# Optimization experiments

Measured on AMD Instinct MI355X. Metric: run time of the kernel, lower is better.

Reference implementation:

```python
import jax, jax.numpy as jnp
import numpy as np

VOCAB, EMB, NDIM, B, T = 50000, 300, 512, 128, 128


def gru_cell(x, h, Wih, Whh, bih, bhh):
    # torch nn.GRU gate order: [r, z, n]
    gi = x @ Wih.T + bih
    gh = h @ Whh.T + bhh
    i_r, i_z, i_n = jnp.split(gi, 3, axis=-1)
    h_r, h_z, h_n = jnp.split(gh, 3, axis=-1)
    r = jax.nn.sigmoid(i_r + h_r)
    z = jax.nn.sigmoid(i_z + h_z)
    n = jnp.tanh(i_n + r * h_n)
    return (1.0 - z) * n + z * h


def masked_gru(X, mask, h0, Wih, Whh, bih, bhh):
    # X: T x B x d, mask: T x B, h0: B x n. Replicates _gru_forward:
    # step-0 output is stored UNmasked (o_tm1 is None), later steps blend.
    h_raw = gru_cell(X[0], h0, Wih, Whh, bih, bhh)
    m0 = mask[0][:, None]
    h = h_raw * m0 + h0 * (1.0 - m0)
    o = h_raw

    def step(carry, inp):
        h, o = carry
        x_t, m_t = inp
        m = m_t[:, None]
        hr = gru_cell(x_t, h, Wih, Whh, bih, bhh)
        h_new = hr * m + h * (1.0 - m)
        o_new = hr * m + o * (1.0 - m)
        return (h_new, o_new), o_new

    (h_f, _), o_rest = jax.lax.scan(step, (h, o), (X[1:], mask[1:]))
    return jnp.concatenate([o[None], o_rest], axis=0), h_f


def rte_forward(premise, hypothesis, E, p_Wih, p_Whh, p_bih, p_bhh,
                h_Wih, h_Whh, h_bih, h_bhh, m_Wih, m_Whh, m_bih, m_bhh,
                W_y, W_h, W_r, W_alpha, out_W, out_b):
    bsz = premise.shape[0]
    n_dim = W_y.shape[0]
    mask_p = (premise != 0).astype(E.dtype).T            # T x B
    mask_h = (hypothesis != 0).astype(E.dtype).T
    enc_p = E[premise].transpose(1, 0, 2)                # T x B x EMB (eval: no dropout)
    enc_h = E[hypothesis].transpose(1, 0, 2)
    h0 = jnp.zeros((bsz, n_dim), dtype=E.dtype)
    o_p, h_n = masked_gru(enc_p, mask_p, h0, p_Wih, p_Whh, p_bih, p_bhh)
    o_h, _ = masked_gru(enc_h, mask_h, h_n, h_Wih, h_Whh, h_bih, h_bhh)

    Y = o_p.transpose(1, 0, 2)                           # B x Tp x n
    Yw = Y @ W_y                                         # hoisted: constant across steps
    maskY = mask_p.T                                     # B x Tp

    def step(r, inp):
        h_t, m_t = inp
        s = h_t @ W_h + r @ W_r                          # B x n
        M = jnp.tanh(Yw + s[:, None, :])                 # B x Tp x n
        alpha = (M @ W_alpha)[..., 0]                    # B x Tp
        alpha = alpha - 1000.0 * (1.0 - maskY)
        alpha = jax.nn.softmax(alpha, axis=-1)
        a = jnp.einsum('bt,btn->bn', alpha, Y)
        m_in = jnp.concatenate([a, h_t], axis=-1)        # B x 2n
        rr = gru_cell(m_in, r, m_Wih, m_Whh, m_bih, m_bhh)
        m = m_t[:, None]
        r_new = rr * m + r * (1.0 - m)
        return r_new, alpha

    r0 = jnp.zeros((bsz, n_dim), dtype=E.dtype)
    r_f, _alpha_vec = jax.lax.scan(step, r0, (o_h, mask_h))
    logits = r_f @ out_W.T + out_b                       # B x 3
    return jax.nn.log_softmax(logits, axis=-1)


def setup_inputs():
    key = jax.random.key(0)
    ks = jax.random.split(key, 22)
    s = 0.05
    def rn(k, sh):
        return jax.random.normal(k, sh, dtype=jnp.float32) * s
    G = 3 * NDIM
    return {
        "premise": jax.random.randint(ks[0], (B, T), 0, VOCAB),
        "hypothesis": jax.random.randint(ks[1], (B, T), 0, VOCAB),
        "E": rn(ks[2], (VOCAB, EMB)),
        "p_Wih": rn(ks[3], (G, EMB)), "p_Whh": rn(ks[4], (G, NDIM)),
        "p_bih": rn(ks[5], (G,)), "p_bhh": rn(ks[6], (G,)),
        "h_Wih": rn(ks[7], (G, EMB)), "h_Whh": rn(ks[8], (G, NDIM)),
        "h_bih": rn(ks[9], (G,)), "h_bhh": rn(ks[10], (G,)),
        "m_Wih": rn(ks[11], (G, 2 * NDIM)), "m_Whh": rn(ks[12], (G, NDIM)),
        "m_bih": rn(ks[13], (G,)), "m_bhh": rn(ks[14], (G,)),
        "W_y": rn(ks[15], (NDIM, NDIM)), "W_h": rn(ks[16], (NDIM, NDIM)),
        "W_r": rn(ks[17], (NDIM, NDIM)), "W_alpha": rn(ks[18], (NDIM, 1)),
        "out_W": rn(ks[19], (3, NDIM)), "out_b": rn(ks[20], (3,)),
    }


def reference(premise, hypothesis, E, p_Wih, p_Whh, p_bih, p_bhh,
              h_Wih, h_Whh, h_bih, h_bhh, m_Wih, m_Whh, m_bih, m_bhh,
              W_y, W_h, W_r, W_alpha, out_W, out_b):
    return rte_forward(premise, hypothesis, E, p_Wih, p_Whh, p_bih, p_bhh,
                       h_Wih, h_Whh, h_bih, h_bhh, m_Wih, m_Whh, m_bih, m_bhh,
                       W_y, W_h, W_r, W_alpha, out_W, out_b)
```

## Files before the change

kernel.cpp:

```cpp
#include <hip/hip_runtime.h>
#include <math.h>

#define B_SZ 128
#define T_SZ 128
#define EMBD 300
#define ND 512
#define G3 1536
#define FPAD 32
#define NFID 320
#define NREP 8

typedef short s16x8 __attribute__((ext_vector_type(8)));
typedef float f32x4 __attribute__((ext_vector_type(4)));
typedef unsigned long long u64;

__device__ __forceinline__ unsigned short f2b(float x) {
    unsigned u = __float_as_uint(x);
    unsigned r = (u + 0x7fff + ((u >> 16) & 1)) >> 16;
    return (unsigned short)r;
}
__device__ __forceinline__ float b2f(unsigned short v) {
    return __uint_as_float(((unsigned)v) << 16);
}
__device__ __forceinline__ float fsigmoid(float x) { return 1.0f / (1.0f + __expf(-x)); }
__device__ __forceinline__ float ftanh(float x) { return 1.0f - 2.0f / (__expf(2.0f * x) + 1.0f); }

__device__ __forceinline__ f32x4 mfma16(s16x8 a, s16x8 b, f32x4 c) {
    return __builtin_amdgcn_mfma_f32_16x16x32_bf16(a, b, c, 0, 0, 0);
}

__device__ __forceinline__ u64 cld64(const void* p) {
    return __hip_atomic_load((const u64*)p, __ATOMIC_RELAXED, __HIP_MEMORY_SCOPE_AGENT);
}
__device__ __forceinline__ void cst64(void* p, u64 v) {
    __hip_atomic_store((u64*)p, v, __ATOMIC_RELAXED, __HIP_MEMORY_SCOPE_AGENT);
}
__device__ __forceinline__ unsigned cld32(const void* p) {
    return __hip_atomic_load((const unsigned*)p, __ATOMIC_RELAXED, __HIP_MEMORY_SCOPE_AGENT);
}
__device__ __forceinline__ void cst32(void* p, unsigned v) {
    __hip_atomic_store((unsigned*)p, v, __ATOMIC_RELAXED, __HIP_MEMORY_SCOPE_AGENT);
}
__device__ __forceinline__ s16x8 cld_frag(const unsigned short* p) {
    union { u64 q[2]; s16x8 v; } u;
    u.q[0] = cld64(p);
    u.q[1] = cld64(p + 4);
    return u.v;
}

__device__ __forceinline__ void postflag(unsigned* flags, int base, int id, unsigned ep)
{
    if (threadIdx.x < NREP)
        cst32(&flags[((long)threadIdx.x * NFID + base + id) * FPAD], ep);
}
__device__ __forceinline__ void waitflags(const unsigned* flags, int base, int n,
                                          unsigned ep, int rep)
{
    const unsigned* fr = flags + (long)rep * NFID * FPAD;
    if (threadIdx.x < 64) {
#pragma unroll 1
        for (int i = threadIdx.x; i < n; i += 64)
            while (cld32(&fr[(long)(base + i) * FPAD]) < ep)
                __builtin_amdgcn_s_sleep(2);
    }
    __syncthreads();
}
__device__ __forceinline__ void fbar(unsigned* flags, int base, int nb, unsigned ep)
{
    __syncthreads();
    postflag(flags, base, blockIdx.x & 63, ep);
    waitflags(flags, base, nb, ep, blockIdx.x & 7);
}

#define FB_GRUP 0
#define FB_GRUH 64
#define FB_LF   128
#define FB_UF   256
#define FB_SF   288

template<typename AT, bool OB>
__global__ __launch_bounds__(256)
void mfma_gemm(const AT* __restrict__ A, const int* __restrict__ idxA,
               const unsigned short* __restrict__ Wb, const float* __restrict__ bias,
               void* __restrict__ Cv,
               int M, int N, int K, int ldA, int Kpad, int ldC, int permC)
{
    __shared__ unsigned short As[64][40];
    __shared__ unsigned short Bs[64][40];
    const int tid = threadIdx.x;
    const int wv = tid >> 6, lane = tid & 63;
    const int wm = wv >> 1, wn = wv & 1;
    const int m0 = blockIdx.y * 64, n0 = blockIdx.x * 64;

    f32x4 acc[2][2] = {{{0.f,0.f,0.f,0.f},{0.f,0.f,0.f,0.f}},
                       {{0.f,0.f,0.f,0.f},{0.f,0.f,0.f,0.f}}};
    const int r_st = tid >> 2, k_st = (tid & 3) * 8;

    long arow = -1;
    {
        int gm = m0 + r_st;
        if (gm < M) arow = idxA ? (long)idxA[gm] : (long)gm;
    }

    const int kIters = (K + 31) / 32;
    for (int it = 0; it < kIters; ++it) {
        const int kg = it * 32 + k_st;
        {
            s16x8 pk = {0,0,0,0,0,0,0,0};
            if (arow >= 0) {
                if constexpr (sizeof(AT) == 2) {
                    if (kg + 8 <= K) {
                        pk = *(const s16x8*)((const unsigned short*)A + arow * (long)ldA + kg);
                    } else {
#pragma unroll
                        for (int j = 0; j < 8; ++j)
                            if (kg + j < K) pk[j] = (short)((const unsigned short*)A)[arow * (long)ldA + kg + j];
                    }
                } else {
                    if (kg + 8 <= K) {
                        const float* p = (const float*)A + arow * (long)ldA + kg;
                        f32x4 u0 = *(const f32x4*)p;
                        f32x4 u1 = *(const f32x4*)(p + 4);
#pragma unroll
                        for (int j = 0; j < 4; ++j) { pk[j] = (short)f2b(u0[j]); pk[4+j] = (short)f2b(u1[j]); }
                    } else {
#pragma unroll
                        for (int j = 0; j < 8; ++j) {
                            int kk = kg + j;
                            if (kk < K) pk[j] = (short)f2b(((const float*)A)[arow * (long)ldA + kk]);
                        }
                    }
                }
            }
            *(s16x8*)&As[r_st][k_st] = pk;
        }
        {
            int gn = n0 + r_st;
            s16x8 pk = {0,0,0,0,0,0,0,0};
            if (gn < N) pk = *(const s16x8*)&Wb[(long)gn * Kpad + kg];
            *(s16x8*)&Bs[r_st][k_st] = pk;
        }
        __syncthreads();
        {
            const int koff = (lane >> 4) * 8;
            s16x8 af[2], bfr[2];
#pragma unroll
            for (int f = 0; f < 2; ++f) {
                af[f]  = *(s16x8*)&As[wm * 32 + f * 16 + (lane & 15)][koff];
                bfr[f] = *(s16x8*)&Bs[wn * 32 + f * 16 + (lane & 15)][koff];
            }
#pragma unroll
            for (int fi = 0; fi < 2; ++fi)
#pragma unroll
                for (int fj = 0; fj < 2; ++fj)
                    acc[fi][fj] = mfma16(af[fi], bfr[fj], acc[fi][fj]);
        }
        __syncthreads();
    }
#pragma unroll
    for (int fi = 0; fi < 2; ++fi)
#pragma unroll
        for (int fj = 0; fj < 2; ++fj)
#pragma unroll
            for (int r = 0; r < 4; ++r) {
                int m = m0 + wm * 32 + fi * 16 + (lane >> 4) * 4 + r;
                int n = n0 + wn * 32 + fj * 16 + (lane & 15);
                if (m < M && n < N) {
                    float v = acc[fi][fj][r];
                    if (bias) v += bias[n];
                    long mo = permC ? ((long)(m & 127) * B_SZ + (m >> 7)) : (long)m;
                    if constexpr (OB) ((unsigned short*)Cv)[mo * ldC + n] = f2b(v);
                    else               ((float*)Cv)[mo * ldC + n] = v;
                }
            }
}

#define GRU_NB 64
__global__ __launch_bounds__(256, 1)
void gru_chain(const unsigned short* __restrict__ Whh_b, const float* __restrict__ GI,
               const float* __restrict__ bhh, const int* __restrict__ toks,
               float* __restrict__ h32,
               unsigned short* __restrict__ h16a, unsigned short* __restrict__ h16b,
               unsigned short* __restrict__ o_bt,
               unsigned* __restrict__ flags, int fbase)
{
    __shared__ unsigned short wlds[3][16][512];
    __shared__ unsigned short ht[64][20];
    const int tid = threadIdx.x;
    const int wv = tid >> 6, lane = tid & 63;
    const int dt = blockIdx.x & 31, bh = blockIdx.x >> 5;
    const int b0 = bh * 64;

    for (int s = 0; s < 12; ++s) {
        int slot = tid + s * 256;
        int g = slot >> 10, rem = slot & 1023, ks = rem >> 6, ln = rem & 63;
        int row = g * ND + dt * 16 + (ln & 15);
        int k = ks * 32 + (ln >> 4) * 8;
        *(s16x8*)&wlds[g][ks][ln * 8] = *(const s16x8*)&Whh_b[(long)row * ND + k];
    }
    __syncthreads();

    const int d = dt * 16 + (lane & 15);
    const int brow = b0 + wv * 16 + (lane >> 4) * 4;
    const long fhrd = ((long)(bh * 4 + wv) * 16) << 9;

    const int bl = tid & 63, dq = tid >> 6;
    const long fhwr = (((long)(bh * 4 + (bl >> 4)) * 16 + (dt >> 1)) << 9)
                    + (((((dt & 1) * 16 + dq * 4) >> 3) * 16 + (bl & 15)) * 8)
                    + (((dt & 1) * 16 + dq * 4) & 7);

    float hreg[4];
#pragma unroll
    for (int rr = 0; rr < 4; ++rr) hreg[rr] = h32[(long)(brow + rr) * ND + d];

    float o_run[4] = {0.f, 0.f, 0.f, 0.f};
    unsigned ep = 0;

    for (int t = 0; t < T_SZ; ++t) {
        const unsigned short* hin16 = (t & 1) ? h16b : h16a;
        unsigned short* hout16 = (t & 1) ? h16a : h16b;

        const float* git = GI + (long)t * (B_SZ * G3);
        float gi_r[4], gi_z[4], gi_n[4]; int mk[4];
#pragma unroll
        for (int rr = 0; rr < 4; ++rr) {
            int b = brow + rr;
            gi_r[rr] = git[(long)b * G3 + d];
            gi_z[rr] = git[(long)b * G3 + ND + d];
            gi_n[rr] = git[(long)b * G3 + 2 * ND + d];
            mk[rr]   = toks[b * T_SZ + t];
        }

        f32x4 acc0 = {0,0,0,0}, acc1 = {0,0,0,0}, acc2 = {0,0,0,0};
#pragma unroll
        for (int ks = 0; ks < 16; ++ks) {
            s16x8 a  = cld_frag(&hin16[fhrd + ((long)ks << 9) + lane * 8]);
            s16x8 br = *(s16x8*)&wlds[0][ks][lane * 8];
            s16x8 bz = *(s16x8*)&wlds[1][ks][lane * 8];
            s16x8 bn = *(s16x8*)&wlds[2][ks][lane * 8];
            acc0 = mfma16(a, br, acc0);
            acc1 = mfma16(a, bz, acc1);
            acc2 = mfma16(a, bn, acc2);
        }

#pragma unroll
        for (int rr = 0; rr < 4; ++rr) {
            int b = brow + rr;
            float rg = fsigmoid(gi_r[rr] + acc0[rr] + bhh[d]);
            float zg = fsigmoid(gi_z[rr] + acc1[rr] + bhh[ND + d]);
            float ng = ftanh(gi_n[rr] + rg * (acc2[rr] + bhh[2 * ND + d]));
            float hr = (1.0f - zg) * ng + zg * hreg[rr];
            bool m = mk[rr] != 0;
            float hn = m ? hr : hreg[rr];
            hreg[rr] = hn;
            ht[b - b0][lane & 15] = f2b(hn);
            if (t == T_SZ - 1) h32[(long)b * ND + d] = hn;
            o_run[rr] = (t == 0) ? hr : (m ? hr : o_run[rr]);
            o_bt[((long)b * T_SZ + t) * ND + d] = f2b(o_run[rr]);
        }
        __syncthreads();
        {
            u64 v = *(u64*)&ht[bl][dq * 4];
            cst64(&hout16[fhwr], v);
        }
        fbar(flags, fbase, GRU_NB, ++ep);
    }
}

#define UP_NB 32
#define YPITCH 536
__global__ __launch_bounds__(256, 1)
void match_chain(const unsigned short* __restrict__ WrT_b,
                 const unsigned short* __restrict__ mWihL_b,
                 const unsigned short* __restrict__ mWhh_b,
                 const unsigned short* __restrict__ OHWh_tb,
                 const unsigned short* __restrict__ OHGI_tb,
                 const float* __restrict__ m_bhh, const float* __restrict__ Walpha,
                 const unsigned short* __restrict__ Yw_bb,
                 const unsigned short* __restrict__ Y_bb,
                 const int* __restrict__ prem, const int* __restrict__ hyp,
                 float* __restrict__ r32,
                 unsigned short* __restrict__ r16a, unsigned short* __restrict__ r16b,
                 unsigned short* __restrict__ a16, unsigned short* __restrict__ s16,
                 unsigned* __restrict__ flags)
{
    __shared__ __align__(16) unsigned char smem[157696];
    const int tid = threadIdx.x;
    const int wv = tid >> 6, lane = tid & 63;

    if (blockIdx.x < 128) {
        const int b = blockIdx.x;
        const int rep = b & 7;
        unsigned short (*ywl)[YPITCH] = (unsigned short(*)[YPITCH])smem;
        float* wal  = (float*)(smem + 137216);
        float* sarr = (float*)(smem + 139264);
        float* part = (float*)(smem + 141312);
        float* lg   = (float*)(smem + 142336);
        float* red  = (float*)(smem + 142848);
        float* sr2  = (float*)(smem + 142880);

        for (int s = 0; s < 32; ++s) {
            int c = s * 256 + tid;
            int row = c >> 6, cg = c & 63;
            *(s16x8*)&ywl[row][cg * 8] =
                *(const s16x8*)&Yw_bb[((long)b * T_SZ + row) * ND + cg * 8];
        }
        if (tid < 128) {
            f32x4 w = *(const f32x4*)&Walpha[tid * 4];
            *(f32x4*)&wal[tid * 4] = w;
        }
        float mmreg = 0.f;
        if (tid < 128) mmreg = (prem[b * T_SZ + tid] != 0) ? 0.f : 1000.f;
        __syncthreads();

        const int tp = tid >> 1, gh = tid & 1;
        const unsigned short* yrow = &ywl[tp][gh * 256];
        const float* sp  = &sarr[gh * 256];
        const float* wap = &wal[gh * 256];
        const int g = tid >> 7, lt = tid & 127, n4 = lt * 4;
        const long fa_wr = (((long)(b >> 4) * 16 + (n4 >> 5)) << 9)
                         + ((((n4 >> 3) & 3) * 16 + (b & 15)) * 8) + (n4 & 7);

        for (int t = 0; t < T_SZ; ++t) {
            waitflags(flags, FB_SF, UP_NB, (unsigned)(t + 1), rep);
            if (tid < 64) {
                s16x8 q = cld_frag(&s16[(long)b * ND + tid * 8]);
#pragma unroll
                for (int j = 0; j < 8; ++j) sarr[tid * 8 + j] = b2f((unsigned short)q[j]);
            }
            __syncthreads();
            {
                float acc = 0.f;
#pragma unroll 4
                for (int i8 = 0; i8 < 32; ++i8) {
                    s16x8 yw = *(const s16x8*)&yrow[i8 * 8];
                    f32x4 s0 = *(const f32x4*)&sp[i8 * 8];
                    f32x4 s1 = *(const f32x4*)&sp[i8 * 8 + 4];
                    f32x4 w0 = *(const f32x4*)&wap[i8 * 8];
                    f32x4 w1 = *(const f32x4*)&wap[i8 * 8 + 4];
#pragma unroll
                    for (int j = 0; j < 4; ++j)
                        acc += ftanh(b2f((unsigned short)yw[j]) + s0[j]) * w0[j];
#pragma unroll
                    for (int j = 0; j < 4; ++j)
                        acc += ftanh(b2f((unsigned short)yw[4 + j]) + s1[j]) * w1[j];
                }
                part[tid] = acc;
            }
            __syncthreads();
            if (tid < 128) lg[tid] = __expf(part[tid * 2] + part[tid * 2 + 1] - mmreg);
            __syncthreads();
            float suml = 0.f;
            f32x4 acw = {0.f, 0.f, 0.f, 0.f};
#pragma unroll 8
            for (int i = 0; i < 64; ++i) {
                int tpp = g * 64 + i;
                float al = lg[tpp];
                suml += al;
                u64 q = *(const u64*)&Y_bb[((long)b * T_SZ + tpp) * ND + n4];
                acw[0] += al * b2f((unsigned short)q);
                acw[1] += al * b2f((unsigned short)(q >> 16));
                acw[2] += al * b2f((unsigned short)(q >> 32));
                acw[3] += al * b2f((unsigned short)(q >> 48));
            }
            if (g == 1) {
                *(f32x4*)&sr2[n4] = acw;
                if (lt == 0) red[0] = suml;
            }
            __syncthreads();
            if (g == 0) {
                float inv = 1.0f / (suml + red[0]);
                f32x4 o = *(f32x4*)&sr2[n4];
                u64 pk = (u64)f2b((acw[0] + o[0]) * inv) | ((u64)f2b((acw[1] + o[1]) * inv) << 16)
                       | ((u64)f2b((acw[2] + o[2]) * inv) << 32) | ((u64)f2b((acw[3] + o[3]) * inv) << 48);
                cst64(&a16[fa_wr], pk);
            }
            __syncthreads();
            postflag(flags, FB_LF, b, (unsigned)(t + 1));
        }
    } else {
        const int ug = blockIdx.x - 128;
        const int rep = ug & 7;
        unsigned short (*wA)[16][512] = (unsigned short(*)[16][512])smem;
        unsigned short (*wR)[16][512] = (unsigned short(*)[16][512])(smem + 49152);
        float (*bounce)[84] = (float(*)[84])(smem + 49152 + 65536);

        for (int s = 0; s < 12; ++s) {
            int slot = tid + s * 256;
            int fam = slot >> 10, rem = slot & 1023, ks = rem >> 6, ln = rem & 63;
            int row = fam * ND + ug * 16 + (ln & 15);
            int k = ks * 32 + (ln >> 4) * 8;
            *(s16x8*)&wA[fam][ks][ln * 8] = *(const s16x8*)&mWihL_b[(long)row * ND + k];
        }
        for (int s = 0; s < 16; ++s) {
            int slot = tid + s * 256;
            int fam = slot >> 10, rem = slot & 1023, ks = rem >> 6, ln = rem & 63;
            int k = ks * 32 + (ln >> 4) * 8;
            const unsigned short* src = (fam < 3)
                ? &mWhh_b[(long)(fam * ND + ug * 16 + (ln & 15)) * ND + k]
                : &WrT_b[(long)(ug * 16 + (ln & 15)) * ND + k];
            *(s16x8*)&wR[fam][ks][ln * 8] = *(const s16x8*)src;
        }
        __syncthreads();

        const int cb = tid >> 1;
        const int half = tid & 1;
        const int d0 = ug * 16 + half * 8;
        const long fr_wr = (((long)(cb >> 4) * 16 + (ug >> 1)) << 9)
                         + ((((d0 >> 3) & 3) * 16 + (cb & 15)) * 8);

        f32x4 rpA = {0,0,0,0}, rpB = {0,0,0,0};

        for (int t = 0; t < T_SZ; ++t) {
            const unsigned short* ohw = &OHWh_tb[((long)t * B_SZ + cb) * ND + d0];
            u64 qa = *(const u64*)ohw;
            u64 qb = *(const u64*)(ohw + 4);
            const unsigned short* og = &OHGI_tb[((long)t * B_SZ + cb) * G3];
            u64 q0a = *(const u64*)&og[d0];            u64 q0b = *(const u64*)&og[d0 + 4];
            u64 q1a = *(const u64*)&og[ND + d0];       u64 q1b = *(const u64*)&og[ND + d0 + 4];
            u64 q2a = *(const u64*)&og[2 * ND + d0];   u64 q2b = *(const u64*)&og[2 * ND + d0 + 4];
            int hv = hyp[cb * T_SZ + t];

            waitflags(flags, FB_UF, UP_NB, (unsigned)t, rep);
            const unsigned short* r16rd = (t & 1) ? r16b : r16a;
            unsigned short*       r16wr = (t & 1) ? r16a : r16b;

            f32x4 aSR[2] = {{0,0,0,0},{0,0,0,0}}, aSZ[2] = {{0,0,0,0},{0,0,0,0}};
            f32x4 aHN[2] = {{0,0,0,0},{0,0,0,0}}, aS[2]  = {{0,0,0,0},{0,0,0,0}};
            f32x4 aGN[2] = {{0,0,0,0},{0,0,0,0}};
#pragma unroll
            for (int f = 0; f < 2; ++f) {
                const long gbase = ((long)(wv * 2 + f) * 16) << 9;
#pragma unroll
                for (int ks = 0; ks < 16; ++ks) {
                    s16x8 a = cld_frag(&r16rd[gbase + ((long)ks << 9) + lane * 8]);
                    aSR[f] = mfma16(a, *(s16x8*)&wR[0][ks][lane * 8], aSR[f]);
                    aSZ[f] = mfma16(a, *(s16x8*)&wR[1][ks][lane * 8], aSZ[f]);
                    aHN[f] = mfma16(a, *(s16x8*)&wR[2][ks][lane * 8], aHN[f]);
                    aS[f]  = mfma16(a, *(s16x8*)&wR[3][ks][lane * 8], aS[f]);
                }
            }
#pragma unroll
            for (int f = 0; f < 2; ++f)
#pragma unroll
                for (int rr = 0; rr < 4; ++rr)
                    bounce[wv * 32 + f * 16 + (lane >> 4) * 4 + rr][64 + (lane & 15)] = aS[f][rr];
            __syncthreads();
            {
                u64 w0 = 0, w1 = 0;
#pragma unroll
                for (int j = 0; j < 4; ++j) {
                    float v0 = bounce[cb][64 + half * 8 + j]     + b2f((unsigned short)(qa >> (16 * j)));
                    float v1 = bounce[cb][64 + half * 8 + 4 + j] + b2f((unsigned short)(qb >> (16 * j)));
                    w0 |= (u64)f2b(v0) << (16 * j);
                    w1 |= (u64)f2b(v1) << (16 * j);
                }
                cst64(&s16[(long)cb * ND + d0], w0);
                cst64(&s16[(long)cb * ND + d0 + 4], w1);
            }
            __syncthreads();
            postflag(flags, FB_SF, ug, (unsigned)(t + 1));

            waitflags(flags, FB_LF, 128, (unsigned)(t + 1), rep);
#pragma unroll
            for (int f = 0; f < 2; ++f) {
                const long gbase = ((long)(wv * 2 + f) * 16) << 9;
#pragma unroll
                for (int ks = 0; ks < 16; ++ks) {
                    s16x8 a = cld_frag(&a16[gbase + ((long)ks << 9) + lane * 8]);
                    aSR[f] = mfma16(a, *(s16x8*)&wA[0][ks][lane * 8], aSR[f]);
                    aSZ[f] = mfma16(a, *(s16x8*)&wA[1][ks][lane * 8], aSZ[f]);
                    aGN[f] = mfma16(a, *(s16x8*)&wA[2][ks][lane * 8], aGN[f]);
                }
            }
#pragma unroll
            for (int f = 0; f < 2; ++f)
#pragma unroll
                for (int rr = 0; rr < 4; ++rr) {
                    int bb = wv * 32 + f * 16 + (lane >> 4) * 4 + rr;
                    bounce[bb][0  + (lane & 15)] = aSR[f][rr];
                    bounce[bb][16 + (lane & 15)] = aSZ[f][rr];
                    bounce[bb][32 + (lane & 15)] = aGN[f][rr];
                    bounce[bb][48 + (lane & 15)] = aHN[f][rr];
                }
            __syncthreads();
            {
                bool mkk = hv != 0;
                u64 w0 = 0, w1 = 0;
#pragma unroll
                for (int j = 0; j < 8; ++j) {
                    int dl = half * 8 + j;
                    int dd = ug * 16 + dl;
                    u64 qg0 = (j < 4) ? q0a : q0b;
                    u64 qg1 = (j < 4) ? q1a : q1b;
                    u64 qg2 = (j < 4) ? q2a : q2b;
                    int sh = 16 * (j & 3);
                    float sr  = bounce[cb][0 + dl]  + b2f((unsigned short)(qg0 >> sh)) + m_bhh[dd];
                    float sz  = bounce[cb][16 + dl] + b2f((unsigned short)(qg1 >> sh)) + m_bhh[ND + dd];
                    float gin = bounce[cb][32 + dl] + b2f((unsigned short)(qg2 >> sh));
                    float ghn = bounce[cb][48 + dl] + m_bhh[2 * ND + dd];
                    float rg = fsigmoid(sr), zg = fsigmoid(sz);
                    float ng = ftanh(gin + rg * ghn);
                    float rp = (j < 4) ? rpA[j & 3] : rpB[j & 3];
                    float rn = (1.0f - zg) * ng + zg * rp;
                    float v = mkk ? rn : rp;
                    if (j < 4) rpA[j & 3] = v; else rpB[j & 3] = v;
                    if (j < 4) w0 |= (u64)f2b(v) << sh; else w1 |= (u64)f2b(v) << sh;
                }
                if (t == T_SZ - 1) {
                    *(f32x4*)&r32[(long)cb * ND + d0] = rpA;
                    *(f32x4*)&r32[(long)cb * ND + d0 + 4] = rpB;
                }
                cst64(&r16wr[fr_wr], w0);
                cst64(&r16wr[fr_wr + 4], w1);
            }
            __syncthreads();
            postflag(flags, FB_UF, ug, (unsigned)(t + 1));
        }
    }
}

__global__ void prep_idx(const int* __restrict__ prem, const int* __restrict__ hyp,
                         int* __restrict__ idx_p, int* __restrict__ idx_h)
{
    int i = blockIdx.x * blockDim.x + threadIdx.x;
    if (i < B_SZ * T_SZ) {
        int t = i / B_SZ, b = i % B_SZ;
        idx_p[i] = prem[b * T_SZ + t];
        idx_h[i] = hyp[b * T_SZ + t];
    }
}

__global__ void conv_w(const float* __restrict__ in, unsigned short* __restrict__ out,
                       int N, int K, int Kpad, int ldIn, int colOff)
{
    long i = (long)blockIdx.x * blockDim.x + threadIdx.x;
    if (i >= (long)N * Kpad) return;
    int n = (int)(i / Kpad), k = (int)(i % Kpad);
    float v = (k < K) ? in[(long)n * ldIn + k + colOff] : 0.0f;
    out[i] = f2b(v);
}

__global__ void conv_wT(const float* __restrict__ in, unsigned short* __restrict__ out,
                        int N, int K, int Kpad, int ldIn)
{
    long i = (long)blockIdx.x * blockDim.x + threadIdx.x;
    if (i >= (long)N * Kpad) return;
    int n = (int)(i / Kpad), k = (int)(i % Kpad);
    float v = (k < K) ? in[(long)k * ldIn + n] : 0.0f;
    out[i] = f2b(v);
}

__global__ void zero_kernel(float* __restrict__ p, int n)
{
    int i = blockIdx.x * blockDim.x + threadIdx.x;
    if (i < n) p[i] = 0.0f;
}

__global__ void final_logits(const float* __restrict__ r, const float* __restrict__ outW,
                             const float* __restrict__ outb, float* __restrict__ out)
{
    int b = blockIdx.x;
    int lane = threadIdx.x;
    float a0 = 0.0f, a1 = 0.0f, a2 = 0.0f;
    for (int k = lane; k < ND; k += 64) {
        float rv = r[(long)b * ND + k];
        a0 += rv * outW[0 * ND + k];
        a1 += rv * outW[1 * ND + k];
        a2 += rv * outW[2 * ND + k];
    }
#pragma unroll
    for (int off = 32; off; off >>= 1) {
        a0 += __shfl_down(a0, off);
        a1 += __shfl_down(a1, off);
        a2 += __shfl_down(a2, off);
    }
    if (lane == 0) {
        float l0 = a0 + outb[0], l1 = a1 + outb[1], l2 = a2 + outb[2];
        float mx = fmaxf(l0, fmaxf(l1, l2));
        float se = expf(l0 - mx) + expf(l1 - mx) + expf(l2 - mx);
        float ls = mx + logf(se);
        out[b * 3 + 0] = l0 - ls;
        out[b * 3 + 1] = l1 - ls;
        out[b * 3 + 2] = l2 - ls;
    }
}

extern "C" void kernel_launch(void* const* d_in, const int* in_sizes, int n_in,
                              void* d_out, int out_size, void* d_ws, size_t ws_size,
                              hipStream_t stream)
{
    const int*   prem    = (const int*)d_in[0];
    const int*   hyp     = (const int*)d_in[1];
    const float* E       = (const float*)d_in[2];
    const float* p_Wih   = (const float*)d_in[3];
    const float* p_Whh   = (const float*)d_in[4];
    const float* p_bih   = (const float*)d_in[5];
    const float* p_bhh   = (const float*)d_in[6];
    const float* h_Wih   = (const float*)d_in[7];
    const float* h_Whh   = (const float*)d_in[8];
    const float* h_bih   = (const float*)d_in[9];
    const float* h_bhh   = (const float*)d_in[10];
    const float* m_Wih   = (const float*)d_in[11];
    const float* m_Whh   = (const float*)d_in[12];
    const float* m_bih   = (const float*)d_in[13];
    const float* m_bhh   = (const float*)d_in[14];
    const float* W_y     = (const float*)d_in[15];
    const float* W_h     = (const float*)d_in[16];
    const float* W_r     = (const float*)d_in[17];
    const float* W_alpha = (const float*)d_in[18];
    const float* out_W   = (const float*)d_in[19];
    const float* out_b   = (const float*)d_in[20];
    float* out = (float*)d_out;

    const int MB = T_SZ * B_SZ;
    const int NFLAGS = NREP * NFID * FPAD;

    float* ws = (float*)d_ws;
    size_t off = 0;
    float* GI    = ws + off; off += (size_t)MB * G3;
    float* h32   = ws + off; off += (size_t)B_SZ * ND;
    float* r32   = ws + off; off += (size_t)B_SZ * ND;
    unsigned* flags = (unsigned*)(ws + off); off += NFLAGS;
    int* idx_p = (int*)(ws + off); off += (size_t)B_SZ * T_SZ;
    int* idx_h = (int*)(ws + off); off += (size_t)B_SZ * T_SZ;
    unsigned short* ub = (unsigned short*)(ws + off);
    size_t uoff = 0;
    unsigned short* o_p_bt = ub + uoff; uoff += (size_t)MB * ND;
    unsigned short* o_h_bt = ub + uoff; uoff += (size_t)MB * ND;
    unsigned short* Yw_bb  = ub + uoff; uoff += (size_t)MB * ND;
    unsigned short* OHWh_tb= ub + uoff; uoff += (size_t)MB * ND;
    unsigned short* OHGI_tb= ub + uoff; uoff += (size_t)MB * G3;
    unsigned short* h16a   = ub + uoff; uoff += (size_t)B_SZ * ND;
    unsigned short* h16b   = ub + uoff; uoff += (size_t)B_SZ * ND;
    unsigned short* r16a   = ub + uoff; uoff += (size_t)B_SZ * ND;
    unsigned short* r16b   = ub + uoff; uoff += (size_t)B_SZ * ND;
    unsigned short* a16    = ub + uoff; uoff += (size_t)B_SZ * ND;
    unsigned short* s16    = ub + uoff; uoff += (size_t)B_SZ * ND;
    unsigned short* pWih_b = ub + uoff; uoff += (size_t)G3 * 320;
    unsigned short* hWih_b = ub + uoff; uoff += (size_t)G3 * 320;
    unsigned short* pWhh_b = ub + uoff; uoff += (size_t)G3 * ND;
    unsigned short* hWhh_b = ub + uoff; uoff += (size_t)G3 * ND;
    unsigned short* mWihL_b= ub + uoff; uoff += (size_t)G3 * ND;
    unsigned short* mWihR  = ub + uoff; uoff += (size_t)G3 * ND;
    unsigned short* mWhh_b = ub + uoff; uoff += (size_t)G3 * ND;
    unsigned short* WyT_b  = ub + uoff; uoff += (size_t)ND * ND;
    unsigned short* WhT_b  = ub + uoff; uoff += (size_t)ND * ND;
    unsigned short* WrT_b  = ub + uoff; uoff += (size_t)ND * ND;
    off += (uoff + 1) / 2;
    if (ws_size < off * sizeof(float)) return;

    auto cblk = [](long n) { return (int)((n + 255) / 256); };

    prep_idx<<<cblk(MB), 256, 0, stream>>>(prem, hyp, idx_p, idx_h);
    conv_w <<<cblk((long)G3 * 320), 256, 0, stream>>>(p_Wih, pWih_b, G3, EMBD, 320, EMBD, 0);
    conv_w <<<cblk((long)G3 * 320), 256, 0, stream>>>(h_Wih, hWih_b, G3, EMBD, 320, EMBD, 0);
    conv_w <<<cblk((long)G3 * ND), 256, 0, stream>>>(p_Whh, pWhh_b, G3, ND, ND, ND, 0);
    conv_w <<<cblk((long)G3 * ND), 256, 0, stream>>>(h_Whh, hWhh_b, G3, ND, ND, ND, 0);
    conv_w <<<cblk((long)G3 * ND), 256, 0, stream>>>(m_Wih, mWihL_b, G3, ND, ND, 2 * ND, 0);
    conv_w <<<cblk((long)G3 * ND), 256, 0, stream>>>(m_Wih, mWihR, G3, ND, ND, 2 * ND, ND);
    conv_w <<<cblk((long)G3 * ND), 256, 0, stream>>>(m_Whh, mWhh_b, G3, ND, ND, ND, 0);
    conv_wT<<<cblk((long)ND * ND), 256, 0, stream>>>(W_y, WyT_b, ND, ND, ND, ND);
    conv_wT<<<cblk((long)ND * ND), 256, 0, stream>>>(W_h, WhT_b, ND, ND, ND, ND);
    conv_wT<<<cblk((long)ND * ND), 256, 0, stream>>>(W_r, WrT_b, ND, ND, ND, ND);
    zero_kernel<<<cblk(B_SZ * ND), 256, 0, stream>>>(h32, B_SZ * ND);
    zero_kernel<<<cblk(B_SZ * ND / 2), 256, 0, stream>>>((float*)h16a, B_SZ * ND / 2);
    zero_kernel<<<cblk(B_SZ * ND), 256, 0, stream>>>(r32, B_SZ * ND);
    zero_kernel<<<cblk(B_SZ * ND / 2), 256, 0, stream>>>((float*)r16a, B_SZ * ND / 2);
    zero_kernel<<<cblk(B_SZ * ND / 2), 256, 0, stream>>>((float*)r16b, B_SZ * ND / 2);
    zero_kernel<<<cblk(NFLAGS), 256, 0, stream>>>((float*)flags, NFLAGS);

    {
        dim3 g(G3 / 64, MB / 64);
        mfma_gemm<float, false><<<g, 256, 0, stream>>>(E, idx_p, pWih_b, p_bih, GI,
                                                       MB, G3, EMBD, EMBD, 320, G3, 0);
    }
    gru_chain<<<GRU_NB, 256, 0, stream>>>(pWhh_b, GI, p_bhh, prem, h32, h16a, h16b,
                                          o_p_bt, flags, FB_GRUP);

    {
        dim3 g(G3 / 64, MB / 64);
        mfma_gemm<float, false><<<g, 256, 0, stream>>>(E, idx_h, hWih_b, h_bih, GI,
                                                       MB, G3, EMBD, EMBD, 320, G3, 0);
    }
    gru_chain<<<GRU_NB, 256, 0, stream>>>(hWhh_b, GI, h_bhh, hyp, h32, h16a, h16b,
                                          o_h_bt, flags, FB_GRUH);

    {
        dim3 g(ND / 64, MB / 64);
        mfma_gemm<unsigned short, true><<<g, 256, 0, stream>>>(o_p_bt, nullptr, WyT_b, nullptr,
                                                               Yw_bb, MB, ND, ND, ND, ND, ND, 0);
        mfma_gemm<unsigned short, true><<<g, 256, 0, stream>>>(o_h_bt, nullptr, WhT_b, nullptr,
                                                               OHWh_tb, MB, ND, ND, ND, ND, ND, 1);
        dim3 g2(G3 / 64, MB / 64);
        mfma_gemm<unsigned short, true><<<g2, 256, 0, stream>>>(o_h_bt, nullptr, mWihR, m_bih,
                                                                OHGI_tb, MB, G3, ND, ND, ND, G3, 1);
    }

    match_chain<<<160, 256, 0, stream>>>(WrT_b, mWihL_b, mWhh_b, OHWh_tb, OHGI_tb,
                                         m_bhh, W_alpha, Yw_bb, o_p_bt, prem, hyp,
                                         r32, r16a, r16b, a16, s16, flags);

    final_logits<<<B_SZ, 64, 0, stream>>>(r32, out_W, out_b, out);
}
```

Baseline: 6.666 ms.

## Replace flag-synchronized match chain with independent per-batch blocks

The attention/match GRU recurrence moves off a cross-block pipeline, where 32 update blocks used MFMA and global flag barriers with 128 attention blocks each step. It now runs as one 512-thread block per batch row that does all matvecs itself with scalar FMA over pre-packed bf16 weights streamed from global/L2. This removes the per-step inter-block flag waits and the global round trips for intermediate vectors. In exchange each block re-reads roughly 3.5 MB of weights every step, without tensor cores, so total L2 bandwidth and ALU work rise sharply.

```diff
diff --git a/kernel.cpp b/kernel.cpp
--- a/kernel.cpp
+++ b/kernel.cpp
@@ -7,7 +7,7 @@
 #define ND 512
 #define G3 1536
 #define FPAD 32
-#define NFID 320
+#define NFID 128
 #define NREP 8
 
 typedef short s16x8 __attribute__((ext_vector_type(8)));
@@ -74,16 +74,13 @@
 
 #define FB_GRUP 0
 #define FB_GRUH 64
-#define FB_LF   128
-#define FB_UF   256
-#define FB_SF   288
 
 template<typename AT, bool OB>
 __global__ __launch_bounds__(256)
 void mfma_gemm(const AT* __restrict__ A, const int* __restrict__ idxA,
                const unsigned short* __restrict__ Wb, const float* __restrict__ bias,
                void* __restrict__ Cv,
-               int M, int N, int K, int ldA, int Kpad, int ldC, int permC)
+               int M, int N, int K, int ldA, int Kpad, int ldC)
 {
     __shared__ unsigned short As[64][40];
     __shared__ unsigned short Bs[64][40];
@@ -168,9 +165,8 @@
                 if (m < M && n < N) {
                     float v = acc[fi][fj][r];
                     if (bias) v += bias[n];
-                    long mo = permC ? ((long)(m & 127) * B_SZ + (m >> 7)) : (long)m;
-                    if constexpr (OB) ((unsigned short*)Cv)[mo * ldC + n] = f2b(v);
-                    else               ((float*)Cv)[mo * ldC + n] = v;
+                    if constexpr (OB) ((unsigned short*)Cv)[(long)m * ldC + n] = f2b(v);
+                    else               ((float*)Cv)[(long)m * ldC + n] = v;
                 }
             }
 }
@@ -267,257 +263,145 @@
     }
 }
 
-#define UP_NB 32
-#define YPITCH 536
-__global__ __launch_bounds__(256, 1)
-void match_chain(const unsigned short* __restrict__ WrT_b,
-                 const unsigned short* __restrict__ mWihL_b,
-                 const unsigned short* __restrict__ mWhh_b,
-                 const unsigned short* __restrict__ OHWh_tb,
-                 const unsigned short* __restrict__ OHGI_tb,
-                 const float* __restrict__ m_bhh, const float* __restrict__ Walpha,
-                 const unsigned short* __restrict__ Yw_bb,
-                 const unsigned short* __restrict__ Y_bb,
-                 const int* __restrict__ prem, const int* __restrict__ hyp,
-                 float* __restrict__ r32,
-                 unsigned short* __restrict__ r16a, unsigned short* __restrict__ r16b,
-                 unsigned short* __restrict__ a16, unsigned short* __restrict__ s16,
-                 unsigned* __restrict__ flags)
-{
-    __shared__ __align__(16) unsigned char smem[157696];
+#define YP 536
+__global__ __launch_bounds__(512, 1)
+void match_pb(const unsigned short* __restrict__ Ws,
+              const unsigned short* __restrict__ Wg,
+              const unsigned short* __restrict__ OHWh_bt,
+              const unsigned short* __restrict__ OHGI_bt,
+              const float* __restrict__ m_bhh, const float* __restrict__ Walpha,
+              const unsigned short* __restrict__ Yw_bb,
+              const unsigned short* __restrict__ Y_bb,
+              const int* __restrict__ prem, const int* __restrict__ hyp,
+              float* __restrict__ r32)
+{
+    __shared__ unsigned short ywl[T_SZ][YP];
+    __shared__ float xv[1024];
+    __shared__ float sarr[512];
+    __shared__ float wal[512];
+    __shared__ float part[512];
+    __shared__ float lg[T_SZ];
+
+    const int b = blockIdx.x;
     const int tid = threadIdx.x;
-    const int wv = tid >> 6, lane = tid & 63;
-
-    if (blockIdx.x < 128) {
-        const int b = blockIdx.x;
-        const int rep = b & 7;
-        unsigned short (*ywl)[YPITCH] = (unsigned short(*)[YPITCH])smem;
-        float* wal  = (float*)(smem + 137216);
-        float* sarr = (float*)(smem + 139264);
-        float* part = (float*)(smem + 141312);
-        float* lg   = (float*)(smem + 142336);
-        float* red  = (float*)(smem + 142848);
-        float* sr2  = (float*)(smem + 142880);
-
-        for (int s = 0; s < 32; ++s) {
-            int c = s * 256 + tid;
-            int row = c >> 6, cg = c & 63;
-            *(s16x8*)&ywl[row][cg * 8] =
-                *(const s16x8*)&Yw_bb[((long)b * T_SZ + row) * ND + cg * 8];
-        }
-        if (tid < 128) {
-            f32x4 w = *(const f32x4*)&Walpha[tid * 4];
-            *(f32x4*)&wal[tid * 4] = w;
-        }
-        float mmreg = 0.f;
-        if (tid < 128) mmreg = (prem[b * T_SZ + tid] != 0) ? 0.f : 1000.f;
-        __syncthreads();
-
-        const int tp = tid >> 1, gh = tid & 1;
-        const unsigned short* yrow = &ywl[tp][gh * 256];
-        const float* sp  = &sarr[gh * 256];
-        const float* wap = &wal[gh * 256];
-        const int g = tid >> 7, lt = tid & 127, n4 = lt * 4;
-        const long fa_wr = (((long)(b >> 4) * 16 + (n4 >> 5)) << 9)
-                         + ((((n4 >> 3) & 3) * 16 + (b & 15)) * 8) + (n4 & 7);
-
-        for (int t = 0; t < T_SZ; ++t) {
-            waitflags(flags, FB_SF, UP_NB, (unsigned)(t + 1), rep);
-            if (tid < 64) {
-                s16x8 q = cld_frag(&s16[(long)b * ND + tid * 8]);
-#pragma unroll
-                for (int j = 0; j < 8; ++j) sarr[tid * 8 + j] = b2f((unsigned short)q[j]);
+
+    for (int s = 0; s < 16; ++s) {
+        int c = s * 512 + tid;
+        int row = c >> 6, cg = c & 63;
+        *(s16x8*)&ywl[row][cg * 8] =
+            *(const s16x8*)&Yw_bb[((long)b * T_SZ + row) * ND + cg * 8];
+    }
+    wal[tid] = Walpha[tid];
+    xv[512 + tid] = 0.0f;
+    float mm = 0.f;
+    if (tid < T_SZ) mm = (prem[b * T_SZ + tid] != 0) ? 0.f : 1000.f;
+    __syncthreads();
+
+    const int tp = tid >> 2, q = tid & 3;
+    const unsigned short* yrow = &ywl[tp][q * 128];
+    const float* sp  = &sarr[q * 128];
+    const float* wap = &wal[q * 128];
+    const unsigned short* ybase = Y_bb + (long)b * T_SZ * ND + tid;
+
+    for (int t = 0; t < T_SZ; ++t) {
+        {
+            float acc = 0.f;
+            const unsigned short* wp = Ws + (long)tid * 8;
+#pragma unroll 4
+            for (int k8 = 0; k8 < 64; ++k8) {
+                f32x4 x0 = *(const f32x4*)&xv[512 + k8 * 8];
+                f32x4 x1 = *(const f32x4*)&xv[512 + k8 * 8 + 4];
+                s16x8 w = *(const s16x8*)(wp + ((long)k8 << 12));
+#pragma unroll
+                for (int j = 0; j < 4; ++j) {
+                    acc += b2f((unsigned short)w[j]) * x0[j];
+                    acc += b2f((unsigned short)w[4 + j]) * x1[j];
+                }
             }
-            __syncthreads();
-            {
-                float acc = 0.f;
+            sarr[tid] = acc + b2f(OHWh_bt[((long)b * T_SZ + t) * ND + tid]);
+        }
+        __syncthreads();
+        {
+            float acc = 0.f;
 #pragma unroll 4
-                for (int i8 = 0; i8 < 32; ++i8) {
-                    s16x8 yw = *(const s16x8*)&yrow[i8 * 8];
-                    f32x4 s0 = *(const f32x4*)&sp[i8 * 8];
-                    f32x4 s1 = *(const f32x4*)&sp[i8 * 8 + 4];
-                    f32x4 w0 = *(const f32x4*)&wap[i8 * 8];
-                    f32x4 w1 = *(const f32x4*)&wap[i8 * 8 + 4];
-#pragma unroll
-                    for (int j = 0; j < 4; ++j)
-                        acc += ftanh(b2f((unsigned short)yw[j]) + s0[j]) * w0[j];
-#pragma unroll
-                    for (int j = 0; j < 4; ++j)
-                        acc += ftanh(b2f((unsigned short)yw[4 + j]) + s1[j]) * w1[j];
-                }
-                part[tid] = acc;
+            for (int i8 = 0; i8 < 16; ++i8) {
+                s16x8 yw = *(const s16x8*)&yrow[i8 * 8];
+                f32x4 s0 = *(const f32x4*)&sp[i8 * 8];
+                f32x4 s1 = *(const f32x4*)&sp[i8 * 8 + 4];
+                f32x4 w0 = *(const f32x4*)&wap[i8 * 8];
+                f32x4 w1 = *(const f32x4*)&wap[i8 * 8 + 4];
+#pragma unroll
+                for (int j = 0; j < 4; ++j)
+                    acc += ftanh(b2f((unsigned short)yw[j]) + s0[j]) * w0[j];
+#pragma unroll
+                for (int j = 0; j < 4; ++j)
+                    acc += ftanh(b2f((unsigned short)yw[4 + j]) + s1[j]) * w1[j];
             }
-            __syncthreads();
-            if (tid < 128) lg[tid] = __expf(part[tid * 2] + part[tid * 2 + 1] - mmreg);
-            __syncthreads();
-            float suml = 0.f;
-            f32x4 acw = {0.f, 0.f, 0.f, 0.f};
+            part[tid] = acc;
+        }
+        __syncthreads();
+        if (tid < T_SZ)
+            lg[tid] = __expf(part[tid * 4] + part[tid * 4 + 1]
+                           + part[tid * 4 + 2] + part[tid * 4 + 3] - mm);
+        __syncthreads();
+        {
+            float suml = 0.f, av = 0.f;
 #pragma unroll 8
-            for (int i = 0; i < 64; ++i) {
-                int tpp = g * 64 + i;
+            for (int tpp = 0; tpp < T_SZ; ++tpp) {
                 float al = lg[tpp];
                 suml += al;
-                u64 q = *(const u64*)&Y_bb[((long)b * T_SZ + tpp) * ND + n4];
-                acw[0] += al * b2f((unsigned short)q);
-                acw[1] += al * b2f((unsigned short)(q >> 16));
-                acw[2] += al * b2f((unsigned short)(q >> 32));
-                acw[3] += al * b2f((unsigned short)(q >> 48));
+                av += al * b2f(ybase[(long)tpp * ND]);
             }
-            if (g == 1) {
-                *(f32x4*)&sr2[n4] = acw;
-                if (lt == 0) red[0] = suml;
-            }
-            __syncthreads();
-            if (g == 0) {
-                float inv = 1.0f / (suml + red[0]);
-                f32x4 o = *(f32x4*)&sr2[n4];
-                u64 pk = (u64)f2b((acw[0] + o[0]) * inv) | ((u64)f2b((acw[1] + o[1]) * inv) << 16)
-                       | ((u64)f2b((acw[2] + o[2]) * inv) << 32) | ((u64)f2b((acw[3] + o[3]) * inv) << 48);
-                cst64(&a16[fa_wr], pk);
-            }
-            __syncthreads();
-            postflag(flags, FB_LF, b, (unsigned)(t + 1));
-        }
-    } else {
-        const int ug = blockIdx.x - 128;
-        const int rep = ug & 7;
-        unsigned short (*wA)[16][512] = (unsigned short(*)[16][512])smem;
-        unsigned short (*wR)[16][512] = (unsigned short(*)[16][512])(smem + 49152);
-        float (*bounce)[84] = (float(*)[84])(smem + 49152 + 65536);
-
-        for (int s = 0; s < 12; ++s) {
-            int slot = tid + s * 256;
-            int fam = slot >> 10, rem = slot & 1023, ks = rem >> 6, ln = rem & 63;
-            int row = fam * ND + ug * 16 + (ln & 15);
-            int k = ks * 32 + (ln >> 4) * 8;
-            *(s16x8*)&wA[fam][ks][ln * 8] = *(const s16x8*)&mWihL_b[(long)row * ND + k];
-        }
-        for (int s = 0; s < 16; ++s) {
-            int slot = tid + s * 256;
-            int fam = slot >> 10, rem = slot & 1023, ks = rem >> 6, ln = rem & 63;
-            int k = ks * 32 + (ln >> 4) * 8;
-            const unsigned short* src = (fam < 3)
-                ? &mWhh_b[(long)(fam * ND + ug * 16 + (ln & 15)) * ND + k]
-                : &WrT_b[(long)(ug * 16 + (ln & 15)) * ND + k];
-            *(s16x8*)&wR[fam][ks][ln * 8] = *(const s16x8*)src;
-        }
-        __syncthreads();
-
-        const int cb = tid >> 1;
-        const int half = tid & 1;
-        const int d0 = ug * 16 + half * 8;
-        const long fr_wr = (((long)(cb >> 4) * 16 + (ug >> 1)) << 9)
-                         + ((((d0 >> 3) & 3) * 16 + (cb & 15)) * 8);
-
-        f32x4 rpA = {0,0,0,0}, rpB = {0,0,0,0};
-
-        for (int t = 0; t < T_SZ; ++t) {
-            const unsigned short* ohw = &OHWh_tb[((long)t * B_SZ + cb) * ND + d0];
-            u64 qa = *(const u64*)ohw;
-            u64 qb = *(const u64*)(ohw + 4);
-            const unsigned short* og = &OHGI_tb[((long)t * B_SZ + cb) * G3];
-            u64 q0a = *(const u64*)&og[d0];            u64 q0b = *(const u64*)&og[d0 + 4];
-            u64 q1a = *(const u64*)&og[ND + d0];       u64 q1b = *(const u64*)&og[ND + d0 + 4];
-            u64 q2a = *(const u64*)&og[2 * ND + d0];   u64 q2b = *(const u64*)&og[2 * ND + d0 + 4];
-            int hv = hyp[cb * T_SZ + t];
-
-            waitflags(flags, FB_UF, UP_NB, (unsigned)t, rep);
-            const unsigned short* r16rd = (t & 1) ? r16b : r16a;
-            unsigned short*       r16wr = (t & 1) ? r16a : r16b;
-
-            f32x4 aSR[2] = {{0,0,0,0},{0,0,0,0}}, aSZ[2] = {{0,0,0,0},{0,0,0,0}};
-            f32x4 aHN[2] = {{0,0,0,0},{0,0,0,0}}, aS[2]  = {{0,0,0,0},{0,0,0,0}};
-            f32x4 aGN[2] = {{0,0,0,0},{0,0,0,0}};
-#pragma unroll
-            for (int f = 0; f < 2; ++f) {
-                const long gbase = ((long)(wv * 2 + f) * 16) << 9;
-#pragma unroll
-                for (int ks = 0; ks < 16; ++ks) {
-                    s16x8 a = cld_frag(&r16rd[gbase + ((long)ks << 9) + lane * 8]);
-                    aSR[f] = mfma16(a, *(s16x8*)&wR[0][ks][lane * 8], aSR[f]);
-                    aSZ[f] = mfma16(a, *(s16x8*)&wR[1][ks][lane * 8], aSZ[f]);
-                    aHN[f] = mfma16(a, *(s16x8*)&wR[2][ks][lane * 8], aHN[f]);
-                    aS[f]  = mfma16(a, *(s16x8*)&wR[3][ks][lane * 8], aS[f]);
+            xv[tid] = av / suml;
+        }
+        __syncthreads();
+        {
+            float aR = 0.f, aZ = 0.f, aGN = 0.f, aHN = 0.f;
+            const unsigned short* wb = Wg + (long)tid * 8;
+#pragma unroll 2
+            for (int k8 = 0; k8 < 64; ++k8) {
+                f32x4 xa0 = *(const f32x4*)&xv[k8 * 8];
+                f32x4 xa1 = *(const f32x4*)&xv[k8 * 8 + 4];
+                f32x4 xr0 = *(const f32x4*)&xv[512 + k8 * 8];
+                f32x4 xr1 = *(const f32x4*)&xv[512 + k8 * 8 + 4];
+                const long ko = (long)k8 << 12;
+                s16x8 wRa = *(const s16x8*)(wb + ko);
+                s16x8 wZa = *(const s16x8*)(wb + ko + (1L << 18));
+                s16x8 wNa = *(const s16x8*)(wb + ko + (2L << 18));
+                s16x8 wRr = *(const s16x8*)(wb + ko + (3L << 18));
+                s16x8 wZr = *(const s16x8*)(wb + ko + (4L << 18));
+                s16x8 wNr = *(const s16x8*)(wb + ko + (5L << 18));
+#pragma unroll
+                for (int j = 0; j < 4; ++j) {
+                    aR  += b2f((unsigned short)wRa[j]) * xa0[j];
+                    aR  += b2f((unsigned short)wRa[4 + j]) * xa1[j];
+                    aZ  += b2f((unsigned short)wZa[j]) * xa0[j];
+                    aZ  += b2f((unsigned short)wZa[4 + j]) * xa1[j];
+                    aGN += b2f((unsigned short)wNa[j]) * xa0[j];
+                    aGN += b2f((unsigned short)wNa[4 + j]) * xa1[j];
+                    aR  += b2f((unsigned short)wRr[j]) * xr0[j];
+                    aR  += b2f((unsigned short)wRr[4 + j]) * xr1[j];
+                    aZ  += b2f((unsigned short)wZr[j]) * xr0[j];
+                    aZ  += b2f((unsigned short)wZr[4 + j]) * xr1[j];
+                    aHN += b2f((unsigned short)wNr[j]) * xr0[j];
+                    aHN += b2f((unsigned short)wNr[4 + j]) * xr1[j];
                 }
             }
-#pragma unroll
-            for (int f = 0; f < 2; ++f)
-#pragma unroll
-                for (int rr = 0; rr < 4; ++rr)
-                    bounce[wv * 32 + f * 16 + (lane >> 4) * 4 + rr][64 + (lane & 15)] = aS[f][rr];
+            const unsigned short* og = OHGI_bt + ((long)b * T_SZ + t) * G3;
+            float rg = fsigmoid(aR + b2f(og[tid]) + m_bhh[tid]);
+            float zg = fsigmoid(aZ + b2f(og[ND + tid]) + m_bhh[ND + tid]);
+            float ng = ftanh(aGN + b2f(og[2 * ND + tid])
+                             + rg * (aHN + m_bhh[2 * ND + tid]));
+            float rp = xv[512 + tid];
+            float rn = (1.0f - zg) * ng + zg * rp;
+            bool mk = hyp[b * T_SZ + t] != 0;
+            float v = mk ? rn : rp;
             __syncthreads();
-            {
-                u64 w0 = 0, w1 = 0;
-#pragma unroll
-                for (int j = 0; j < 4; ++j) {
-                    float v0 = bounce[cb][64 + half * 8 + j]     + b2f((unsigned short)(qa >> (16 * j)));
-                    float v1 = bounce[cb][64 + half * 8 + 4 + j] + b2f((unsigned short)(qb >> (16 * j)));
-                    w0 |= (u64)f2b(v0) << (16 * j);
-                    w1 |= (u64)f2b(v1) << (16 * j);
-                }
-                cst64(&s16[(long)cb * ND + d0], w0);
-                cst64(&s16[(long)cb * ND + d0 + 4], w1);
-            }
-            __syncthreads();
-            postflag(flags, FB_SF, ug, (unsigned)(t + 1));
-
-            waitflags(flags, FB_LF, 128, (unsigned)(t + 1), rep);
-#pragma unroll
-            for (int f = 0; f < 2; ++f) {
-                const long gbase = ((long)(wv * 2 + f) * 16) << 9;
-#pragma unroll
-                for (int ks = 0; ks < 16; ++ks) {
-                    s16x8 a = cld_frag(&a16[gbase + ((long)ks << 9) + lane * 8]);
-                    aSR[f] = mfma16(a, *(s16x8*)&wA[0][ks][lane * 8], aSR[f]);
-                    aSZ[f] = mfma16(a, *(s16x8*)&wA[1][ks][lane * 8], aSZ[f]);
-                    aGN[f] = mfma16(a, *(s16x8*)&wA[2][ks][lane * 8], aGN[f]);
-                }
-            }
-#pragma unroll
-            for (int f = 0; f < 2; ++f)
-#pragma unroll
-                for (int rr = 0; rr < 4; ++rr) {
-                    int bb = wv * 32 + f * 16 + (lane >> 4) * 4 + rr;
-                    bounce[bb][0  + (lane & 15)] = aSR[f][rr];
-                    bounce[bb][16 + (lane & 15)] = aSZ[f][rr];
-                    bounce[bb][32 + (lane & 15)] = aGN[f][rr];
-                    bounce[bb][48 + (lane & 15)] = aHN[f][rr];
-                }
-            __syncthreads();
-            {
-                bool mkk = hv != 0;
-                u64 w0 = 0, w1 = 0;
-#pragma unroll
-                for (int j = 0; j < 8; ++j) {
-                    int dl = half * 8 + j;
-                    int dd = ug * 16 + dl;
-                    u64 qg0 = (j < 4) ? q0a : q0b;
-                    u64 qg1 = (j < 4) ? q1a : q1b;
-                    u64 qg2 = (j < 4) ? q2a : q2b;
-                    int sh = 16 * (j & 3);
-                    float sr  = bounce[cb][0 + dl]  + b2f((unsigned short)(qg0 >> sh)) + m_bhh[dd];
-                    float sz  = bounce[cb][16 + dl] + b2f((unsigned short)(qg1 >> sh)) + m_bhh[ND + dd];
-                    float gin = bounce[cb][32 + dl] + b2f((unsigned short)(qg2 >> sh));
-                    float ghn = bounce[cb][48 + dl] + m_bhh[2 * ND + dd];
-                    float rg = fsigmoid(sr), zg = fsigmoid(sz);
-                    float ng = ftanh(gin + rg * ghn);
-                    float rp = (j < 4) ? rpA[j & 3] : rpB[j & 3];
-                    float rn = (1.0f - zg) * ng + zg * rp;
-                    float v = mkk ? rn : rp;
-                    if (j < 4) rpA[j & 3] = v; else rpB[j & 3] = v;
-                    if (j < 4) w0 |= (u64)f2b(v) << sh; else w1 |= (u64)f2b(v) << sh;
-                }
-                if (t == T_SZ - 1) {
-                    *(f32x4*)&r32[(long)cb * ND + d0] = rpA;
-                    *(f32x4*)&r32[(long)cb * ND + d0 + 4] = rpB;
-                }
-                cst64(&r16wr[fr_wr], w0);
-                cst64(&r16wr[fr_wr + 4], w1);
-            }
-            __syncthreads();
-            postflag(flags, FB_UF, ug, (unsigned)(t + 1));
-        }
-    }
+            xv[512 + tid] = v;
+        }
+        __syncthreads();
+    }
+    r32[(long)b * ND + tid] = xv[512 + tid];
 }
 
 __global__ void prep_idx(const int* __restrict__ prem, const int* __restrict__ hyp,
@@ -548,6 +432,29 @@
     if (i >= (long)N * Kpad) return;
     int n = (int)(i / Kpad), k = (int)(i % Kpad);
     float v = (k < K) ? in[(long)k * ldIn + n] : 0.0f;
+    out[i] = f2b(v);
+}
+
+__global__ void pack_ws(const float* __restrict__ Wr, unsigned short* __restrict__ out)
+{
+    long i = (long)blockIdx.x * blockDim.x + threadIdx.x;
+    if (i >= 64L * 512 * 8) return;
+    int k8 = (int)(i >> 12), n = (int)((i >> 3) & 511), j = (int)(i & 7);
+    out[i] = f2b(Wr[(long)(k8 * 8 + j) * ND + n]);
+}
+
+__global__ void pack_wg(const float* __restrict__ mWih, const float* __restrict__ mWhh,
+                        unsigned short* __restrict__ out)
+{
+    long i = (long)blockIdx.x * blockDim.x + threadIdx.x;
+    if (i >= 6L * 64 * 512 * 8) return;
+    int fam = (int)(i >> 18);
+    long rem = i & 262143;
+    int k8 = (int)(rem >> 12), n = (int)((rem >> 3) & 511), j = (int)(rem & 7);
+    int k = k8 * 8 + j;
+    float v;
+    if (fam < 3) v = mWih[(long)(fam * ND + n) * 1024 + k];
+    else         v = mWhh[(long)((fam - 3) * ND + n) * ND + k];
     out[i] = f2b(v);
 }
 
@@ -629,24 +536,19 @@
     unsigned short* o_p_bt = ub + uoff; uoff += (size_t)MB * ND;
     unsigned short* o_h_bt = ub + uoff; uoff += (size_t)MB * ND;
     unsigned short* Yw_bb  = ub + uoff; uoff += (size_t)MB * ND;
-    unsigned short* OHWh_tb= ub + uoff; uoff += (size_t)MB * ND;
-    unsigned short* OHGI_tb= ub + uoff; uoff += (size_t)MB * G3;
+    unsigned short* OHWh_bt= ub + uoff; uoff += (size_t)MB * ND;
+    unsigned short* OHGI_bt= ub + uoff; uoff += (size_t)MB * G3;
     unsigned short* h16a   = ub + uoff; uoff += (size_t)B_SZ * ND;
     unsigned short* h16b   = ub + uoff; uoff += (size_t)B_SZ * ND;
-    unsigned short* r16a   = ub + uoff; uoff += (size_t)B_SZ * ND;
-    unsigned short* r16b   = ub + uoff; uoff += (size_t)B_SZ * ND;
-    unsigned short* a16    = ub + uoff; uoff += (size_t)B_SZ * ND;
-    unsigned short* s16    = ub + uoff; uoff += (size_t)B_SZ * ND;
     unsigned short* pWih_b = ub + uoff; uoff += (size_t)G3 * 320;
     unsigned short* hWih_b = ub + uoff; uoff += (size_t)G3 * 320;
     unsigned short* pWhh_b = ub + uoff; uoff += (size_t)G3 * ND;
     unsigned short* hWhh_b = ub + uoff; uoff += (size_t)G3 * ND;
-    unsigned short* mWihL_b= ub + uoff; uoff += (size_t)G3 * ND;
     unsigned short* mWihR  = ub + uoff; uoff += (size_t)G3 * ND;
-    unsigned short* mWhh_b = ub + uoff; uoff += (size_t)G3 * ND;
     unsigned short* WyT_b  = ub + uoff; uoff += (size_t)ND * ND;
     unsigned short* WhT_b  = ub + uoff; uoff += (size_t)ND * ND;
-    unsigned short* WrT_b  = ub + uoff; uoff += (size_t)ND * ND;
+    unsigned short* Ws_p   = ub + uoff; uoff += 64L * 512 * 8;
+    unsigned short* Wg_p   = ub + uoff; uoff += 6L * 64 * 512 * 8;
     off += (uoff + 1) / 2;
     if (ws_size < off * sizeof(float)) return;
 
@@ -657,23 +559,19 @@
     conv_w <<<cblk((long)G3 * 320), 256, 0, stream>>>(h_Wih, hWih_b, G3, EMBD, 320, EMBD, 0);
     conv_w <<<cblk((long)G3 * ND), 256, 0, stream>>>(p_Whh, pWhh_b, G3, ND, ND, ND, 0);
     conv_w <<<cblk((long)G3 * ND), 256, 0, stream>>>(h_Whh, hWhh_b, G3, ND, ND, ND, 0);
-    conv_w <<<cblk((long)G3 * ND), 256, 0, stream>>>(m_Wih, mWihL_b, G3, ND, ND, 2 * ND, 0);
     conv_w <<<cblk((long)G3 * ND), 256, 0, stream>>>(m_Wih, mWihR, G3, ND, ND, 2 * ND, ND);
-    conv_w <<<cblk((long)G3 * ND), 256, 0, stream>>>(m_Whh, mWhh_b, G3, ND, ND, ND, 0);
     conv_wT<<<cblk((long)ND * ND), 256, 0, stream>>>(W_y, WyT_b, ND, ND, ND, ND);
     conv_wT<<<cblk((long)ND * ND), 256, 0, stream>>>(W_h, WhT_b, ND, ND, ND, ND);
-    conv_wT<<<cblk((long)ND * ND), 256, 0, stream>>>(W_r, WrT_b, ND, ND, ND, ND);
+    pack_ws<<<cblk(64L * 512 * 8), 256, 0, stream>>>(W_r, Ws_p);
+    pack_wg<<<cblk(6L * 64 * 512 * 8), 256, 0, stream>>>(m_Wih, m_Whh, Wg_p);
     zero_kernel<<<cblk(B_SZ * ND), 256, 0, stream>>>(h32, B_SZ * ND);
     zero_kernel<<<cblk(B_SZ * ND / 2), 256, 0, stream>>>((float*)h16a, B_SZ * ND / 2);
-    zero_kernel<<<cblk(B_SZ * ND), 256, 0, stream>>>(r32, B_SZ * ND);
-    zero_kernel<<<cblk(B_SZ * ND / 2), 256, 0, stream>>>((float*)r16a, B_SZ * ND / 2);
-    zero_kernel<<<cblk(B_SZ * ND / 2), 256, 0, stream>>>((float*)r16b, B_SZ * ND / 2);
     zero_kernel<<<cblk(NFLAGS), 256, 0, stream>>>((float*)flags, NFLAGS);
 
     {
         dim3 g(G3 / 64, MB / 64);
         mfma_gemm<float, false><<<g, 256, 0, stream>>>(E, idx_p, pWih_b, p_bih, GI,
-                                                       MB, G3, EMBD, EMBD, 320, G3, 0);
+                                                       MB, G3, EMBD, EMBD, 320, G3);
     }
     gru_chain<<<GRU_NB, 256, 0, stream>>>(pWhh_b, GI, p_bhh, prem, h32, h16a, h16b,
                                           o_p_bt, flags, FB_GRUP);
@@ -681,7 +579,7 @@
     {
         dim3 g(G3 / 64, MB / 64);
         mfma_gemm<float, false><<<g, 256, 0, stream>>>(E, idx_h, hWih_b, h_bih, GI,
-                                                       MB, G3, EMBD, EMBD, 320, G3, 0);
+                                                       MB, G3, EMBD, EMBD, 320, G3);
     }
     gru_chain<<<GRU_NB, 256, 0, stream>>>(hWhh_b, GI, h_bhh, hyp, h32, h16a, h16b,
                                           o_h_bt, flags, FB_GRUH);
@@ -689,17 +587,16 @@
     {
         dim3 g(ND / 64, MB / 64);
         mfma_gemm<unsigned short, true><<<g, 256, 0, stream>>>(o_p_bt, nullptr, WyT_b, nullptr,
-                                                               Yw_bb, MB, ND, ND, ND, ND, ND, 0);
+                                                               Yw_bb, MB, ND, ND, ND, ND, ND);
         mfma_gemm<unsigned short, true><<<g, 256, 0, stream>>>(o_h_bt, nullptr, WhT_b, nullptr,
-                                                               OHWh_tb, MB, ND, ND, ND, ND, ND, 1);
+                                                               OHWh_bt, MB, ND, ND, ND, ND, ND);
         dim3 g2(G3 / 64, MB / 64);
         mfma_gemm<unsigned short, true><<<g2, 256, 0, stream>>>(o_h_bt, nullptr, mWihR, m_bih,
-                                                                OHGI_tb, MB, G3, ND, ND, ND, G3, 1);
-    }
-
-    match_chain<<<160, 256, 0, stream>>>(WrT_b, mWihL_b, mWhh_b, OHWh_tb, OHGI_tb,
-                                         m_bhh, W_alpha, Yw_bb, o_p_bt, prem, hyp,
-                                         r32, r16a, r16b, a16, s16, flags);
+                                                                OHGI_bt, MB, G3, ND, ND, ND, G3);
+    }
+
+    match_pb<<<B_SZ, 512, 0, stream>>>(Ws_p, Wg_p, OHWh_bt, OHGI_bt, m_bhh, W_alpha,
+                                       Yw_bb, o_p_bt, prem, hyp, r32);
 
     final_logits<<<B_SZ, 64, 0, stream>>>(r32, out_W, out_b, out);
 }
```

Result: slower. 8.128 ms (+21.9%).
